# Performance work log

Hardware: AMD Instinct MI355X
Metric: run time of the kernel (lower is better)

## Reference

```python
import jax, jax.numpy as jnp
import numpy as np

EPS = 1e-5

def group_norm(x, gamma, beta, groups):
    # x: (B, C, D, H, W)
    B, C = x.shape[0], x.shape[1]
    xr = x.reshape(B, groups, C // groups, -1)
    mean = xr.mean(axis=(2, 3), keepdims=True)
    var = xr.var(axis=(2, 3), keepdims=True)
    xn = ((xr - mean) * jax.lax.rsqrt(var + EPS)).reshape(x.shape)
    return xn * gamma[None, :, None, None, None] + beta[None, :, None, None, None]

def setup_inputs() -> dict:
    key = jax.random.key(0)
    ks = jax.random.split(key, 8)
    B, Ccls = 2, 32
    D = H = W = 64
    s = 0.05
    return {
        "x": jax.random.normal(ks[0], (B, 768, 8, 8, 8), jnp.float32),
        "out": jax.random.normal(ks[1], (B, 48, D, H, W), jnp.float32),
        "task_encoding": jax.random.normal(ks[2], (Ccls, 256, 1, 1, 1), jnp.float32),
        "gn1_g": jnp.ones((768,), jnp.float32),
        "gn1_b": jnp.zeros((768,), jnp.float32),
        "gap_w": jax.random.normal(ks[3], (256, 768), jnp.float32) * s,
        "gap_b": jnp.zeros((256,), jnp.float32),
        "ctrl_w": jax.random.normal(ks[4], (153, 512), jnp.float32) * s,
        "ctrl_b": jnp.zeros((153,), jnp.float32),
        "gn2_g": jnp.ones((48,), jnp.float32),
        "gn2_b": jnp.zeros((48,), jnp.float32),
        "pre_w": jax.random.normal(ks[5], (8, 48), jnp.float32) * s,
        "pre_b": jnp.zeros((8,), jnp.float32),
    }

def reference(x, out, task_encoding, gn1_g, gn1_b, gap_w, gap_b, ctrl_w, ctrl_b,
              gn2_g, gn2_b, pre_w, pre_b):
    B = x.shape[0]
    Ccls = task_encoding.shape[0]
    # GAP branch: GroupNorm(16,768) -> ReLU -> global avg pool -> 1x1x1 conv 768->256
    h = jax.nn.relu(group_norm(x, gn1_g, gn1_b, 16))
    pooled = h.mean(axis=(2, 3, 4))                       # (B, 768)
    x_feat = pooled @ gap_w.T + gap_b                     # (B, 256)
    # Controller: per (batch, class) params from concat(x_feat, task_encoding)
    te = task_encoding.reshape(Ccls, -1)                  # (Ccls, 256)
    params = (jnp.einsum('pf,bf->bp', ctrl_w[:, :256], x_feat)[:, None, :]
              + jnp.einsum('pf,cf->cp', ctrl_w[:, 256:], te)[None, :, :]
              + ctrl_b)                                   # (B, Ccls, 153)
    w1 = params[..., 0:64].reshape(B, Ccls, 8, 8)
    w2 = params[..., 64:128].reshape(B, Ccls, 8, 8)
    w3 = params[..., 128:136].reshape(B, Ccls, 1, 8)
    b1 = params[..., 136:144]
    b2 = params[..., 144:152]
    b3 = params[..., 152:153]
    # precls branch: GroupNorm(16,48) -> ReLU -> 1x1x1 conv 48->8
    g = jax.nn.relu(group_norm(out, gn2_g, gn2_b, 16))
    h0 = jnp.einsum('oc,bcdhw->bodhw', pre_w, g) + pre_b[None, :, None, None, None]
    # Dynamic per-class head: 8->8->8->1 pointwise MLP with ReLU between layers
    t = jax.nn.relu(jnp.einsum('bcij,bjdhw->bcidhw', w1, h0) + b1[..., None, None, None])
    t = jax.nn.relu(jnp.einsum('bcij,bcjdhw->bcidhw', w2, t) + b2[..., None, None, None])
    logits = jnp.einsum('bcij,bcjdhw->bcidhw', w3, t) + b3[..., None, None, None]
    # (B, Ccls, 1, D, H, W) -> (B, Ccls, D, H, W)
    return logits[:, :, 0]
```

## Files before the change

kernel.cpp:

```cpp
#include <hip/hip_runtime.h>

constexpr int NCLS = 32;

constexpr int WS_POOL = 64;
constexpr int WS_XF  = 1600;
constexpr int WS_PAR = 2112;
constexpr int WS_P2  = 11904;

typedef float f2 __attribute__((ext_vector_type(2)));

__device__ __forceinline__ float wred(float v) {
#pragma unroll
  for (int off = 32; off > 0; off >>= 1) v += __shfl_down(v, off, 64);
  return v;
}

__device__ __forceinline__ f2 pfma(float w, f2 v, f2 a) {
  return __builtin_elementwise_fma((f2)w, v, a);
}
__device__ __forceinline__ f2 paff(f2 v, float sc, float sh) {
  return __builtin_elementwise_fma(v, (f2)sc, (f2)sh);
}
__device__ __forceinline__ f2 prelu(f2 a) {
  return __builtin_elementwise_max(a, (f2)0.f);
}

__global__ void k1_stats(const float* __restrict__ x, const float* __restrict__ oin,
                         const float* __restrict__ g1, const float* __restrict__ b1,
                         float* __restrict__ ws) {
  int t = threadIdx.x;
  int wid = t >> 6, lane = t & 63;
  __shared__ float red[8];
  if (blockIdx.x < 768) {
    int blk = blockIdx.x;
    const float4* p = reinterpret_cast<const float4*>(oin + (size_t)blk * 32768);
    float s = 0.f, s2 = 0.f;
#pragma unroll
    for (int k = 0; k < 32; ++k) {
      float4 v = p[k * 256 + t];
      s  += v.x + v.y + v.z + v.w;
      s2 += v.x*v.x + v.y*v.y + v.z*v.z + v.w*v.w;
    }
    s = wred(s); s2 = wred(s2);
    if (lane == 0) { red[wid*2] = s; red[wid*2+1] = s2; }
    __syncthreads();
    if (t == 0) {
      ws[WS_P2 + blk*2]   = red[0]+red[2]+red[4]+red[6];
      ws[WS_P2 + blk*2+1] = red[1]+red[3]+red[5]+red[7];
    }
  } else {
    int g = blockIdx.x - 768;
    __shared__ float mstat[2];
    const float4* p = reinterpret_cast<const float4*>(x + g * 24576);
    float s = 0.f, s2 = 0.f;
#pragma unroll
    for (int k = 0; k < 24; ++k) {
      float4 v = p[k * 256 + t];
      s  += v.x + v.y + v.z + v.w;
      s2 += v.x*v.x + v.y*v.y + v.z*v.z + v.w*v.w;
    }
    s = wred(s); s2 = wred(s2);
    if (lane == 0) { red[wid*2] = s; red[wid*2+1] = s2; }
    __syncthreads();
    if (t == 0) {
      float S  = red[0]+red[2]+red[4]+red[6];
      float S2 = red[1]+red[3]+red[5]+red[7];
      float mean = S * (1.f/24576.f);
      float var  = S2 * (1.f/24576.f) - mean*mean;
      mstat[0] = mean; mstat[1] = rsqrtf(var + 1e-5f);
    }
    __syncthreads();
    float mean = mstat[0], rstd = mstat[1];
#pragma unroll
    for (int k = 0; k < 12; ++k) {
      int i = k*4 + wid;
      int c = (g & 15) * 48 + i;
      float sc = rstd * g1[c];
      float sh = b1[c] - mean * sc;
      const float* q = x + g * 24576 + i * 512;
      float acc = 0.f;
#pragma unroll
      for (int j = 0; j < 8; ++j)
        acc += fmaxf(fmaf(q[lane + j*64], sc, sh), 0.f);
      acc = wred(acc);
      if (lane == 0) ws[WS_POOL + (g >> 4) * 768 + c] = acc * (1.f/512.f);
    }
  }
}

__global__ void k2_xfeat(const float* __restrict__ gapw, const float* __restrict__ gapb,
                         float* __restrict__ ws) {
  int wid = threadIdx.x >> 6, lane = threadIdx.x & 63;
  int idx = blockIdx.x * 4 + wid;
  int b = idx >> 8, o = idx & 255;
  const float* pw = gapw + o * 768;
  const float* pp = ws + WS_POOL + b * 768;
  float s = 0.f;
#pragma unroll
  for (int i = 0; i < 12; ++i) {
    int cc = lane + i*64;
    s += pw[cc] * pp[cc];
  }
  s = wred(s);
  if (lane == 0) ws[WS_XF + idx] = s + gapb[o];
}

__global__ void k3_params(const float* __restrict__ cw, const float* __restrict__ cb,
                          const float* __restrict__ te, float* __restrict__ ws) {
  int wid = threadIdx.x >> 6, lane = threadIdx.x & 63;
  int e = blockIdx.x * 4 + wid;
  int b = e / (NCLS * 153);
  int r = e % (NCLS * 153);
  int c = r / 153, p = r % 153;
  const float* w  = cw + p * 512;
  const float* xf = ws + WS_XF + b * 256;
  const float* tv = te + c * 256;
  float s = 0.f;
#pragma unroll
  for (int i = 0; i < 4; ++i) {
    int f = lane + i*64;
    s += w[f] * xf[f] + w[256 + f] * tv[f];
  }
  s = wred(s);
  if (lane == 0) ws[WS_PAR + e] = s + cb[p];
}

__global__ __launch_bounds__(256) void k4_main(const float* __restrict__ oin,
                                               const float* __restrict__ prew,
                                               const float* __restrict__ preb,
                                               const float* __restrict__ g2,
                                               const float* __restrict__ b2,
                                               const float* __restrict__ ws,
                                               float* __restrict__ out) {
  __shared__ __align__(16) float Wl[16 * 160];
  __shared__ __align__(16) float prewT[384];
  __shared__ float2 ssl[48];
  __shared__ float ms[64];
  int t = threadIdx.x;
  int b    = blockIdx.x >> 8;
  int rem  = blockIdx.x & 255;
  int tile = rem >> 1;
  int cls0 = (rem & 1) << 4;

  if (t < 32) {
    float S = 0.f, S2 = 0.f;
#pragma unroll
    for (int k = 0; k < 24; ++k) {
      S  += ws[WS_P2 + (t*24 + k)*2];
      S2 += ws[WS_P2 + (t*24 + k)*2 + 1];
    }
    float mean = S * (1.f/786432.f);
    float var  = S2 * (1.f/786432.f) - mean*mean;
    ms[t*2] = mean; ms[t*2+1] = rsqrtf(var + 1e-5f);
  }
  if (t < 128) {
#pragma unroll
    for (int k = 0; k < 3; ++k) {
      int i = t + k*128;
      prewT[(i % 48) * 8 + (i / 48)] = prew[i];
    }
  }
  {
    const float* wsrc = ws + WS_PAR + (size_t)(b * NCLS + cls0) * 153;
#pragma unroll 4
    for (int cc = 0; cc < 16; ++cc)
      if (t < 153) Wl[cc*160 + t] = wsrc[cc*153 + t];
  }
  __syncthreads();
  if (t < 48) {
    int grp = (b << 4) + t / 3;
    float mean = ms[grp*2], rstd = ms[grp*2+1];
    float sc = rstd * g2[t];
    ssl[t] = make_float2(sc, b2[t] - mean * sc);
  }
  __syncthreads();

  const float4* ip4 = reinterpret_cast<const float4*>(oin)
                      + (size_t)b * 48 * 65536 + tile*512 + t;
  const float4* pT4 = reinterpret_cast<const float4*>(prewT);
  f2 h0[8][4];
#pragma unroll
  for (int o = 0; o < 8; ++o) {
    float pb = preb[o];
#pragma unroll
    for (int p = 0; p < 4; ++p) h0[o][p] = (f2)pb;
  }
#pragma unroll 8
  for (int c = 0; c < 48; ++c) {
    float4 va = ip4[(size_t)c * 65536];
    float4 vb = ip4[(size_t)c * 65536 + 256];
    float2 ss = ssl[c];
    f2 g[4];
    g[0] = prelu(paff((f2){va.x, va.y}, ss.x, ss.y));
    g[1] = prelu(paff((f2){va.z, va.w}, ss.x, ss.y));
    g[2] = prelu(paff((f2){vb.x, vb.y}, ss.x, ss.y));
    g[3] = prelu(paff((f2){vb.z, vb.w}, ss.x, ss.y));
    float4 w0 = pT4[c*2], w1 = pT4[c*2+1];
    float wv[8] = {w0.x, w0.y, w0.z, w0.w, w1.x, w1.y, w1.z, w1.w};
#pragma unroll
    for (int o = 0; o < 8; ++o)
#pragma unroll
      for (int p = 0; p < 4; ++p) h0[o][p] = pfma(wv[o], g[p], h0[o][p]);
  }

  float4* op4 = reinterpret_cast<float4*>(out)
                + (size_t)(b * NCLS + cls0) * 65536 + tile*512 + t;
#pragma unroll 1
  for (int cls = 0; cls < 16; ++cls) {
    const float*  Wc = Wl + cls * 160;
    const float4* W4 = reinterpret_cast<const float4*>(Wc);
    float4 b1q0 = W4[34], b1q1 = W4[35];
    float4 b2q0 = W4[36], b2q1 = W4[37];
    float4 w3q0 = W4[32], w3q1 = W4[33];
    float b3v = Wc[152];
    float b1arr[8] = {b1q0.x,b1q0.y,b1q0.z,b1q0.w,b1q1.x,b1q1.y,b1q1.z,b1q1.w};
    float b2arr[8] = {b2q0.x,b2q0.y,b2q0.z,b2q0.w,b2q1.x,b2q1.y,b2q1.z,b2q1.w};
    float w3arr[8] = {w3q0.x,w3q0.y,w3q0.z,w3q0.w,w3q1.x,w3q1.y,w3q1.z,w3q1.w};

    f2 t1[8][4];
#pragma unroll
    for (int i = 0; i < 8; ++i) {
      float4 w0 = W4[i*2], w1 = W4[i*2+1];
      float wv[8] = {w0.x, w0.y, w0.z, w0.w, w1.x, w1.y, w1.z, w1.w};
      f2 a[4];
#pragma unroll
      for (int p = 0; p < 4; ++p) a[p] = (f2)b1arr[i];
#pragma unroll
      for (int j = 0; j < 8; ++j)
#pragma unroll
        for (int p = 0; p < 4; ++p) a[p] = pfma(wv[j], h0[j][p], a[p]);
#pragma unroll
      for (int p = 0; p < 4; ++p) t1[i][p] = prelu(a[p]);
    }
    f2 lg[4];
#pragma unroll
    for (int p = 0; p < 4; ++p) lg[p] = (f2)b3v;
#pragma unroll
    for (int i = 0; i < 8; ++i) {
      float4 w0 = W4[16 + i*2], w1 = W4[17 + i*2];
      float wv[8] = {w0.x, w0.y, w0.z, w0.w, w1.x, w1.y, w1.z, w1.w};
      f2 a[4];
#pragma unroll
      for (int p = 0; p < 4; ++p) a[p] = (f2)b2arr[i];
#pragma unroll
      for (int j = 0; j < 8; ++j)
#pragma unroll
        for (int p = 0; p < 4; ++p) a[p] = pfma(wv[j], t1[j][p], a[p]);
#pragma unroll
      for (int p = 0; p < 4; ++p) {
        a[p] = prelu(a[p]);
        lg[p] = pfma(w3arr[i], a[p], lg[p]);
      }
    }
    op4[(size_t)cls * 65536]       = make_float4(lg[0].x, lg[0].y, lg[1].x, lg[1].y);
    op4[(size_t)cls * 65536 + 256] = make_float4(lg[2].x, lg[2].y, lg[3].x, lg[3].y);
  }
}

extern "C" void kernel_launch(void* const* d_in, const int* in_sizes, int n_in,
                              void* d_out, int out_size, void* d_ws, size_t ws_size,
                              hipStream_t stream) {
  const float* x    = (const float*)d_in[0];
  const float* oin  = (const float*)d_in[1];
  const float* te   = (const float*)d_in[2];
  const float* g1   = (const float*)d_in[3];
  const float* b1   = (const float*)d_in[4];
  const float* gapw = (const float*)d_in[5];
  const float* gapb = (const float*)d_in[6];
  const float* cw   = (const float*)d_in[7];
  const float* cb   = (const float*)d_in[8];
  const float* g2   = (const float*)d_in[9];
  const float* b2   = (const float*)d_in[10];
  const float* prew = (const float*)d_in[11];
  const float* preb = (const float*)d_in[12];
  float* ws  = (float*)d_ws;
  float* out = (float*)d_out;

  hipLaunchKernelGGL(k1_stats,  dim3(800),  dim3(256), 0, stream, x, oin, g1, b1, ws);
  hipLaunchKernelGGL(k2_xfeat,  dim3(128),  dim3(256), 0, stream, gapw, gapb, ws);
  hipLaunchKernelGGL(k3_params, dim3(2448), dim3(256), 0, stream, cw, cb, te, ws);
  hipLaunchKernelGGL(k4_main,   dim3(512),  dim3(256), 0, stream, oin, prew, preb, g2, b2, ws, out);
}
```

Before: 281.8 us.

## Process all classes per block and read dynamic weights from global memory

Each block of k4_main now handles all 32 classes for its tile instead of 16, which halves the grid and removes the duplicated read and GroupNorm/pre-conv pass over the 48-channel input. The per-class MLP weights are read straight from the workspace with uniform scalar loads rather than being staged in LDS. The cost is half as many blocks (256 on a large GPU), so occupancy and latency hiding drop, and the per-class loop doubles in length.

```diff
diff --git a/kernel.cpp b/kernel.cpp
--- a/kernel.cpp
+++ b/kernel.cpp
@@ -132,15 +132,12 @@
                                                const float* __restrict__ b2,
                                                const float* __restrict__ ws,
                                                float* __restrict__ out) {
-  __shared__ __align__(16) float Wl[16 * 160];
   __shared__ __align__(16) float prewT[384];
   __shared__ float2 ssl[48];
   __shared__ float ms[64];
   int t = threadIdx.x;
-  int b    = blockIdx.x >> 8;
-  int rem  = blockIdx.x & 255;
-  int tile = rem >> 1;
-  int cls0 = (rem & 1) << 4;
+  int b    = blockIdx.x >> 7;
+  int tile = blockIdx.x & 127;
 
   if (t < 32) {
     float S = 0.f, S2 = 0.f;
@@ -159,12 +156,6 @@
       int i = t + k*128;
       prewT[(i % 48) * 8 + (i / 48)] = prew[i];
     }
-  }
-  {
-    const float* wsrc = ws + WS_PAR + (size_t)(b * NCLS + cls0) * 153;
-#pragma unroll 4
-    for (int cc = 0; cc < 16; ++cc)
-      if (t < 153) Wl[cc*160 + t] = wsrc[cc*153 + t];
   }
   __syncthreads();
   if (t < 48) {
@@ -203,53 +194,49 @@
       for (int p = 0; p < 4; ++p) h0[o][p] = pfma(wv[o], g[p], h0[o][p]);
   }
 
+  const float* __restrict__ Wb = ws + WS_PAR + (size_t)b * NCLS * 153;
   float4* op4 = reinterpret_cast<float4*>(out)
-                + (size_t)(b * NCLS + cls0) * 65536 + tile*512 + t;
+                + (size_t)b * NCLS * 65536 + tile*512 + t;
 #pragma unroll 1
-  for (int cls = 0; cls < 16; ++cls) {
-    const float*  Wc = Wl + cls * 160;
-    const float4* W4 = reinterpret_cast<const float4*>(Wc);
-    float4 b1q0 = W4[34], b1q1 = W4[35];
-    float4 b2q0 = W4[36], b2q1 = W4[37];
-    float4 w3q0 = W4[32], w3q1 = W4[33];
+  for (int cls = 0; cls < NCLS; ++cls) {
+    const float* Wc = Wb + cls * 153;
+    f2 t1[8][4];
+#pragma unroll
+    for (int i = 0; i < 8; ++i) {
+      float bi = Wc[136 + i];
+      f2 a[4];
+#pragma unroll
+      for (int p = 0; p < 4; ++p) a[p] = (f2)bi;
+#pragma unroll
+      for (int j = 0; j < 8; ++j) {
+        float w = Wc[i*8 + j];
+#pragma unroll
+        for (int p = 0; p < 4; ++p) a[p] = pfma(w, h0[j][p], a[p]);
+      }
+#pragma unroll
+      for (int p = 0; p < 4; ++p) t1[i][p] = prelu(a[p]);
+    }
     float b3v = Wc[152];
-    float b1arr[8] = {b1q0.x,b1q0.y,b1q0.z,b1q0.w,b1q1.x,b1q1.y,b1q1.z,b1q1.w};
-    float b2arr[8] = {b2q0.x,b2q0.y,b2q0.z,b2q0.w,b2q1.x,b2q1.y,b2q1.z,b2q1.w};
-    float w3arr[8] = {w3q0.x,w3q0.y,w3q0.z,w3q0.w,w3q1.x,w3q1.y,w3q1.z,w3q1.w};
-
-    f2 t1[8][4];
+    f2 lg[4];
+#pragma unroll
+    for (int p = 0; p < 4; ++p) lg[p] = (f2)b3v;
 #pragma unroll
     for (int i = 0; i < 8; ++i) {
-      float4 w0 = W4[i*2], w1 = W4[i*2+1];
-      float wv[8] = {w0.x, w0.y, w0.z, w0.w, w1.x, w1.y, w1.z, w1.w};
+      float bi = Wc[144 + i];
       f2 a[4];
 #pragma unroll
-      for (int p = 0; p < 4; ++p) a[p] = (f2)b1arr[i];
-#pragma unroll
-      for (int j = 0; j < 8; ++j)
-#pragma unroll
-        for (int p = 0; p < 4; ++p) a[p] = pfma(wv[j], h0[j][p], a[p]);
-#pragma unroll
-      for (int p = 0; p < 4; ++p) t1[i][p] = prelu(a[p]);
-    }
-    f2 lg[4];
-#pragma unroll
-    for (int p = 0; p < 4; ++p) lg[p] = (f2)b3v;
-#pragma unroll
-    for (int i = 0; i < 8; ++i) {
-      float4 w0 = W4[16 + i*2], w1 = W4[17 + i*2];
-      float wv[8] = {w0.x, w0.y, w0.z, w0.w, w1.x, w1.y, w1.z, w1.w};
-      f2 a[4];
-#pragma unroll
-      for (int p = 0; p < 4; ++p) a[p] = (f2)b2arr[i];
-#pragma unroll
-      for (int j = 0; j < 8; ++j)
-#pragma unroll
-        for (int p = 0; p < 4; ++p) a[p] = pfma(wv[j], t1[j][p], a[p]);
+      for (int p = 0; p < 4; ++p) a[p] = (f2)bi;
+#pragma unroll
+      for (int j = 0; j < 8; ++j) {
+        float w = Wc[64 + i*8 + j];
+#pragma unroll
+        for (int p = 0; p < 4; ++p) a[p] = pfma(w, t1[j][p], a[p]);
+      }
+      float w3 = Wc[128 + i];
 #pragma unroll
       for (int p = 0; p < 4; ++p) {
         a[p] = prelu(a[p]);
-        lg[p] = pfma(w3arr[i], a[p], lg[p]);
+        lg[p] = pfma(w3, a[p], lg[p]);
       }
     }
     op4[(size_t)cls * 65536]       = make_float4(lg[0].x, lg[0].y, lg[1].x, lg[1].y);
@@ -279,5 +266,5 @@
   hipLaunchKernelGGL(k1_stats,  dim3(800),  dim3(256), 0, stream, x, oin, g1, b1, ws);
   hipLaunchKernelGGL(k2_xfeat,  dim3(128),  dim3(256), 0, stream, gapw, gapb, ws);
   hipLaunchKernelGGL(k3_params, dim3(2448), dim3(256), 0, stream, cw, cb, te, ws);
-  hipLaunchKernelGGL(k4_main,   dim3(512),  dim3(256), 0, stream, oin, prew, preb, g2, b2, ws, out);
-}
+  hipLaunchKernelGGL(k4_main,   dim3(256),  dim3(256), 0, stream, oin, prew, preb, g2, b2, ws, out);
+}
```

Result: slower. 305.3 us (+8.4%).
